# Performance work log

Measured on AMD Instinct MI355X. Metric: run time of the kernel, lower is better.

## Reference

```python
import jax, jax.numpy as jnp
import numpy as np

B = 256
NUM_CAPS = 2            # digit capsules
N_IN = 6 * 6 * 6 * 32   # 6912 input capsules
D_OUT = 16
D_IN = 8
N_ROUTING = 3           # original loops range(3 - 1) = 2 iterations
EPS = 1e-9


def squash(s):
    # squash along last axis: (|s|^2/(1+|s|^2)) * s/|s|
    n2 = jnp.sum(s * s, axis=-1, keepdims=True)
    return (n2 / (1.0 + n2)) * s / jnp.sqrt(n2 + EPS)


def setup_inputs() -> dict:
    key = jax.random.key(0)
    k1, k2 = jax.random.split(key)
    x = jax.random.normal(k1, (B, N_IN, D_IN), dtype=jnp.float32)
    W = jax.random.normal(k2, (NUM_CAPS, N_IN, D_OUT, D_IN), dtype=jnp.float32) * 0.1
    return {"x": x, "W": W}


def reference(x, W):
    # tile x over the 2 digit capsules + per-(capsule, input-capsule) matvec:
    # u_hat[b,j,n,e] = sum_d W[j,n,e,d] * x[b,n,d]   -> [B, 2, N, 16]
    u_hat = jnp.einsum('bnd,jned->bjne', x, W)
    b_logits = jnp.zeros(u_hat.shape[:3], dtype=x.dtype)  # [B, 2, N]
    v = None
    for _ in range(N_ROUTING - 1):
        c = jax.nn.softmax(b_logits, axis=1)               # softmax over the 2 capsules (dim=1 in source)
        s = jnp.einsum('bjn,bjne->bje', c, u_hat)          # [B, 2, 16]
        v = squash(s)
        b_logits = b_logits + jnp.einsum('bje,bjne->bjn', v, u_hat)
    return v
```

## Files before the change

kernel.cpp:

```cpp
#include <hip/hip_runtime.h>

#define B_ 256
#define J_ 2
#define N_ 6912
#define E_ 16
#define D_ 8
#define NPW 9
#define NB 36
#define CGX 192


__global__ __launch_bounds__(256, 3) void kpass1(const float* __restrict__ x,
                                                 const float* __restrict__ W,
                                                 float* __restrict__ partial)
{
  __shared__ float smem[9216];
  const int tid  = threadIdx.x;
  const int lane = tid & 63;
  const int wv   = __builtin_amdgcn_readfirstlane(tid >> 6);
  const int b    = blockIdx.y*64 + lane;
  const int nb0  = blockIdx.x * NB;

  const float* xp = x + ((size_t)b*N_ + nb0 + wv*NPW)*D_;
  float4 pa0 = *(const float4*)(xp + 0);
  float4 pb0 = *(const float4*)(xp + 4);
  float4 pa1 = *(const float4*)(xp + 8);
  float4 pb1 = *(const float4*)(xp + 12);

  float4 wbuf[9];
  #pragma unroll
  for (int k=0;k<9;++k){
    const int idx = k*256 + tid;
    const int j   = (idx >= 1152) ? 1 : 0;
    const int r4  = idx - j*1152;
    wbuf[k] = *(const float4*)(W + ((size_t)j*N_ + nb0)*(E_*D_) + (size_t)r4*4);
  }
  #pragma unroll
  for (int k=0;k<9;++k)
    *(float4*)(smem + (size_t)(k*256 + tid)*4) = wbuf[k];
  __syncthreads();

  float acc[32];
  #pragma unroll
  for (int i=0;i<32;++i) acc[i]=0.f;

  #pragma unroll 1
  for (int ni=0; ni<9; ++ni){
    const float4 va = pa0, vb = pb0;
    pa0 = pa1; pb0 = pb1;
    if (ni < 7){
      pa1 = *(const float4*)(xp + (ni+2)*8);
      pb1 = *(const float4*)(xp + (ni+2)*8 + 4);
    }
    const int nl = wv*NPW + ni;
    #pragma unroll
    for (int j=0;j<J_;++j){
      const float* wp = smem + (j*NB + nl)*(E_*D_);
      #pragma unroll
      for (int e=0;e<E_;++e){
        const float4 wa = *(const float4*)(wp + e*8);
        const float4 wb = *(const float4*)(wp + e*8 + 4);
        float a = acc[j*16+e];
        a = fmaf(wa.x, va.x, a); a = fmaf(wa.y, va.y, a);
        a = fmaf(wa.z, va.z, a); a = fmaf(wa.w, va.w, a);
        a = fmaf(wb.x, vb.x, a); a = fmaf(wb.y, vb.y, a);
        a = fmaf(wb.z, vb.z, a); a = fmaf(wb.w, vb.w, a);
        acc[j*16+e] = a;
      }
    }
  }

  __syncthreads();
  #pragma unroll
  for (int i=0;i<32;++i) smem[tid*33 + i] = acc[i];
  __syncthreads();
  const int bl = tid >> 2;
  const int i0 = (tid & 3) * 8;
  float v[8];
  #pragma unroll
  for (int k=0;k<8;++k){
    float s = 0.f;
    #pragma unroll
    for (int w=0; w<4; ++w) s += smem[(w*64 + bl)*33 + i0 + k];
    v[k] = s;
  }
  float* dst = partial + (size_t)(blockIdx.x*4 + blockIdx.y)*2048 + bl*32 + i0;
  *(float4*)(dst)     = make_float4(v[0],v[1],v[2],v[3]);
  *(float4*)(dst + 4) = make_float4(v[4],v[5],v[6],v[7]);
}

__global__ __launch_bounds__(256, 3) void kpass2(const float* __restrict__ x,
                                                 const float* __restrict__ W,
                                                 const float* __restrict__ v1,
                                                 float* __restrict__ partial)
{
  __shared__ float smem[9216];
  const int tid  = threadIdx.x;
  const int lane = tid & 63;
  const int wv   = __builtin_amdgcn_readfirstlane(tid >> 6);
  const int b    = blockIdx.y*64 + lane;
  const int nb0  = blockIdx.x * NB;

  const float* xp = x + ((size_t)b*N_ + nb0 + wv*NPW)*D_;
  float4 pa0 = *(const float4*)(xp + 0);
  float4 pb0 = *(const float4*)(xp + 4);
  float4 pa1 = *(const float4*)(xp + 8);
  float4 pb1 = *(const float4*)(xp + 12);

  float4 wbuf[9];
  #pragma unroll
  for (int k=0;k<9;++k){
    const int idx = k*256 + tid;
    const int j   = (idx >= 1152) ? 1 : 0;
    const int r4  = idx - j*1152;
    wbuf[k] = *(const float4*)(W + ((size_t)j*N_ + nb0)*(E_*D_) + (size_t)r4*4);
  }
  #pragma unroll
  for (int k=0;k<9;++k)
    *(float4*)(smem + (size_t)(k*256 + tid)*4) = wbuf[k];

  float vv[32];
  {
    const float4* vp = (const float4*)(v1 + (size_t)b*32);
    #pragma unroll
    for (int q=0;q<8;++q){
      const float4 t4 = vp[q];
      vv[q*4+0]=t4.x; vv[q*4+1]=t4.y; vv[q*4+2]=t4.z; vv[q*4+3]=t4.w;
    }
  }
  __syncthreads();

  float acc[32];
  #pragma unroll
  for (int i=0;i<32;++i) acc[i]=0.f;

  #pragma unroll 1
  for (int ni=0; ni<9; ++ni){
    const float4 va = pa0, vb = pb0;
    pa0 = pa1; pb0 = pb1;
    if (ni < 7){
      pa1 = *(const float4*)(xp + (ni+2)*8);
      pb1 = *(const float4*)(xp + (ni+2)*8 + 4);
    }
    const int nl = wv*NPW + ni;
    float u[32];
    #pragma unroll
    for (int j=0;j<J_;++j){
      const float* wp = smem + (j*NB + nl)*(E_*D_);
      #pragma unroll
      for (int e=0;e<E_;++e){
        const float4 wa = *(const float4*)(wp + e*8);
        const float4 wb = *(const float4*)(wp + e*8 + 4);
        float a;
        a = wa.x*va.x;           a = fmaf(wa.y, va.y, a);
        a = fmaf(wa.z, va.z, a); a = fmaf(wa.w, va.w, a);
        a = fmaf(wb.x, vb.x, a); a = fmaf(wb.y, vb.y, a);
        a = fmaf(wb.z, vb.z, a); a = fmaf(wb.w, vb.w, a);
        u[j*16+e] = a;
      }
    }
    float l0=0.f, l1=0.f;
    #pragma unroll
    for (int e=0;e<E_;++e){
      l0 = fmaf(vv[e],    u[e],    l0);
      l1 = fmaf(vv[16+e], u[16+e], l1);
    }
    const float c0 = 1.f/(1.f + __expf(l1 - l0));
    const float c1 = 1.f - c0;
    #pragma unroll
    for (int e=0;e<E_;++e){
      acc[e]    = fmaf(c0, u[e],    acc[e]);
      acc[16+e] = fmaf(c1, u[16+e], acc[16+e]);
    }
  }

  __syncthreads();
  #pragma unroll
  for (int i=0;i<32;++i) smem[tid*33 + i] = acc[i];
  __syncthreads();
  const int bl = tid >> 2;
  const int i0 = (tid & 3) * 8;
  float v[8];
  #pragma unroll
  for (int k=0;k<8;++k){
    float s = 0.f;
    #pragma unroll
    for (int w=0; w<4; ++w) s += smem[(w*64 + bl)*33 + i0 + k];
    v[k] = s;
  }
  float* dst = partial + (size_t)(blockIdx.x*4 + blockIdx.y)*2048 + bl*32 + i0;
  *(float4*)(dst)     = make_float4(v[0],v[1],v[2],v[3]);
  *(float4*)(dst + 4) = make_float4(v[4],v[5],v[6],v[7]);
}

template<bool HALF>
__global__ __launch_bounds__(256) void kred(const float* __restrict__ partial,
                                            float* __restrict__ dst)
{
  const int t = blockIdx.x*256 + threadIdx.x;
  const int btile = t >> 11, q = t & 2047;
  const float* p = partial + (size_t)btile*2048 + q;
  float s = 0.f;
  #pragma unroll 8
  for (int cx=0; cx<CGX; ++cx) s += p[(size_t)cx*8192];
  if (HALF) s *= 0.5f;
  float n2 = s*s;
  #pragma unroll
  for (int m=1; m<16; m<<=1) n2 += __shfl_xor(n2, m);
  const float f = (n2/(1.f+n2)) * rsqrtf(n2 + 1e-9f);
  dst[t] = s * f;
}

#define NT 512
__global__ __launch_bounds__(NT) void kmono(const float* __restrict__ x,
                                            const float* __restrict__ W,
                                            float* __restrict__ out)
{
  const int b    = blockIdx.x;
  const int tid  = threadIdx.x;
  const int wv   = tid >> 6;
  const int lane = tid & 63;
  __shared__ float wred[8*33];
  __shared__ float vsh[32];

  float acc[32];
  #pragma unroll
  for (int i=0;i<32;++i) acc[i]=0.f;
  for (int n = tid; n < N_; n += NT){
    const float4 xa = *(const float4*)(x + ((size_t)b*N_ + n)*D_);
    const float4 xb = *(const float4*)(x + ((size_t)b*N_ + n)*D_ + 4);
    #pragma unroll
    for (int j=0;j<J_;++j){
      const float* wp = W + ((size_t)j*N_ + n)*(E_*D_);
      #pragma unroll
      for (int e=0;e<E_;++e){
        const float4 wa = *(const float4*)(wp + e*8);
        const float4 wb = *(const float4*)(wp + e*8 + 4);
        float a = acc[j*16+e];
        a = fmaf(wa.x,xa.x,a); a = fmaf(wa.y,xa.y,a); a = fmaf(wa.z,xa.z,a); a = fmaf(wa.w,xa.w,a);
        a = fmaf(wb.x,xb.x,a); a = fmaf(wb.y,xb.y,a); a = fmaf(wb.z,xb.z,a); a = fmaf(wb.w,xb.w,a);
        acc[j*16+e] = a;
      }
    }
  }
  #pragma unroll
  for (int i=0;i<32;++i){
    float v = acc[i];
    #pragma unroll
    for (int off=32; off; off>>=1) v += __shfl_xor(v, off);
    acc[i] = v;
  }
  if (lane == 0){
    #pragma unroll
    for (int i=0;i<32;++i) wred[wv*33 + i] = acc[i];
  }
  __syncthreads();
  if (tid < 32){
    float s = 0.f;
    #pragma unroll
    for (int w=0;w<8;++w) s += wred[w*33 + tid];
    wred[tid] = 0.5f * s;
  }
  __syncthreads();
  if (tid < 32){
    const int j = tid >> 4; float n2 = 0.f;
    #pragma unroll
    for (int e=0;e<16;++e){ const float sv = wred[j*16+e]; n2 = fmaf(sv,sv,n2); }
    vsh[tid] = wred[tid] * (n2/(1.f+n2)) * rsqrtf(n2 + 1e-9f);
  }
  __syncthreads();
  float vv[32];
  #pragma unroll
  for (int i=0;i<32;++i) vv[i] = vsh[i];

  #pragma unroll
  for (int i=0;i<32;++i) acc[i]=0.f;
  for (int n = tid; n < N_; n += NT){
    const float4 xa = *(const float4*)(x + ((size_t)b*N_ + n)*D_);
    const float4 xb = *(const float4*)(x + ((size_t)b*N_ + n)*D_ + 4);
    float u[32];
    #pragma unroll
    for (int j=0;j<J_;++j){
      const float* wp = W + ((size_t)j*N_ + n)*(E_*D_);
      #pragma unroll
      for (int e=0;e<E_;++e){
        const float4 wa = *(const float4*)(wp + e*8);
        const float4 wb = *(const float4*)(wp + e*8 + 4);
        float a;
        a = wa.x*xa.x; a = fmaf(wa.y,xa.y,a); a = fmaf(wa.z,xa.z,a); a = fmaf(wa.w,xa.w,a);
        a = fmaf(wb.x,xb.x,a); a = fmaf(wb.y,xb.y,a); a = fmaf(wb.z,xb.z,a); a = fmaf(wb.w,xb.w,a);
        u[j*16+e] = a;
      }
    }
    float l0=0.f, l1=0.f;
    #pragma unroll
    for (int e=0;e<16;++e){ l0 = fmaf(vv[e],u[e],l0); l1 = fmaf(vv[16+e],u[16+e],l1); }
    const float c0 = 1.f/(1.f + __expf(l1 - l0));
    const float c1 = 1.f - c0;
    #pragma unroll
    for (int e=0;e<16;++e){ acc[e] = fmaf(c0,u[e],acc[e]); acc[16+e] = fmaf(c1,u[16+e],acc[16+e]); }
  }
  #pragma unroll
  for (int i=0;i<32;++i){
    float v = acc[i];
    #pragma unroll
    for (int off=32; off; off>>=1) v += __shfl_xor(v, off);
    acc[i] = v;
  }
  __syncthreads();
  if (lane == 0){
    #pragma unroll
    for (int i=0;i<32;++i) wred[wv*33 + i] = acc[i];
  }
  __syncthreads();
  if (tid < 32){
    float s = 0.f;
    #pragma unroll
    for (int w=0;w<8;++w) s += wred[w*33 + tid];
    wred[tid] = s;
  }
  __syncthreads();
  if (tid < 32){
    const int j = tid >> 4; float n2 = 0.f;
    #pragma unroll
    for (int e=0;e<16;++e){ const float sv = wred[j*16+e]; n2 = fmaf(sv,sv,n2); }
    out[(size_t)b*32 + tid] = wred[tid] * (n2/(1.f+n2)) * rsqrtf(n2 + 1e-9f);
  }
}

extern "C" void kernel_launch(void* const* d_in, const int* in_sizes, int n_in,
                              void* d_out, int out_size, void* d_ws, size_t ws_size,
                              hipStream_t stream)
{
  const float* x = (const float*)d_in[0];
  const float* W = (const float*)d_in[1];
  if (n_in >= 2 && in_sizes[0] < in_sizes[1]){
    x = (const float*)d_in[1]; W = (const float*)d_in[0];
  }
  float* out = (float*)d_out;

  const size_t need_main = (size_t)(8192 + 768*2048) * sizeof(float);

  if (ws_size >= need_main){
    float* wsf     = (float*)d_ws;
    float* v1      = wsf;
    float* partial = wsf + 8192;
    kpass1<<<dim3(CGX,4), 256, 0, stream>>>(x, W, partial);
    kred<true ><<<32, 256, 0, stream>>>(partial, v1);
    kpass2<<<dim3(CGX,4), 256, 0, stream>>>(x, W, v1, partial);
    kred<false><<<32, 256, 0, stream>>>(partial, out);
  } else {
    kmono<<<B_, NT, 0, stream>>>(x, W, out);
  }
}
```

Measured before the change: 162.7 us.

## Remap threads to output element and batch so each wave covers all input capsules

Threads are reassigned so that each lane owns one output element e for 4 batch rows, and each wave walks all 36 input capsules of the block, instead of each lane owning a batch row with 32 accumulators over 9 capsules per wave. This drops the cross-wave shared-memory reduction and its barriers and lowers register pressure. In pass 2 the agreement dot product over e becomes a DPP row reduction across 16 lanes, and the divide becomes a fast reciprocal. The cost is that x rows are now loaded redundantly by 16 lanes (broadcast loads), and the per-iteration shared-memory weight reads are strided by e, which may cause bank conflicts.

```diff
diff --git a/kernel.cpp b/kernel.cpp
--- a/kernel.cpp
+++ b/kernel.cpp
@@ -5,9 +5,17 @@
 #define N_ 6912
 #define E_ 16
 #define D_ 8
-#define NPW 9
 #define NB 36
 #define CGX 192
+#define BSTR (4*N_*D_)
+
+__device__ __forceinline__ float dpp_row_add16(float v){
+  v += __int_as_float(__builtin_amdgcn_update_dpp(0, __float_as_int(v), 0xB1,  0xF, 0xF, true));
+  v += __int_as_float(__builtin_amdgcn_update_dpp(0, __float_as_int(v), 0x4E,  0xF, 0xF, true));
+  v += __int_as_float(__builtin_amdgcn_update_dpp(0, __float_as_int(v), 0x141, 0xF, 0xF, true));
+  v += __int_as_float(__builtin_amdgcn_update_dpp(0, __float_as_int(v), 0x140, 0xF, 0xF, true));
+  return v;
+}
 
 
 __global__ __launch_bounds__(256, 3) void kpass1(const float* __restrict__ x,
@@ -18,14 +26,9 @@
   const int tid  = threadIdx.x;
   const int lane = tid & 63;
   const int wv   = __builtin_amdgcn_readfirstlane(tid >> 6);
-  const int b    = blockIdx.y*64 + lane;
+  const int e    = lane & 15;
+  const int blo  = lane >> 4;
   const int nb0  = blockIdx.x * NB;
-
-  const float* xp = x + ((size_t)b*N_ + nb0 + wv*NPW)*D_;
-  float4 pa0 = *(const float4*)(xp + 0);
-  float4 pb0 = *(const float4*)(xp + 4);
-  float4 pa1 = *(const float4*)(xp + 8);
-  float4 pb1 = *(const float4*)(xp + 12);
 
   float4 wbuf[9];
   #pragma unroll
@@ -38,55 +41,58 @@
   #pragma unroll
   for (int k=0;k<9;++k)
     *(float4*)(smem + (size_t)(k*256 + tid)*4) = wbuf[k];
-  __syncthreads();
-
-  float acc[32];
-  #pragma unroll
-  for (int i=0;i<32;++i) acc[i]=0.f;
-
+
+  const int b0 = blockIdx.y*64 + wv*16 + blo;
+  const float* xp = x + ((size_t)b0*N_ + nb0)*D_;
+
+  float4 xa[4], xb[4];
+  #pragma unroll
+  for (int k=0;k<4;++k){
+    xa[k] = *(const float4*)(xp + (size_t)k*BSTR);
+    xb[k] = *(const float4*)(xp + (size_t)k*BSTR + 4);
+  }
+  __syncthreads();
+
+  float acc0[4] = {0,0,0,0}, acc1[4] = {0,0,0,0};
   #pragma unroll 1
-  for (int ni=0; ni<9; ++ni){
-    const float4 va = pa0, vb = pb0;
-    pa0 = pa1; pb0 = pb1;
-    if (ni < 7){
-      pa1 = *(const float4*)(xp + (ni+2)*8);
-      pb1 = *(const float4*)(xp + (ni+2)*8 + 4);
-    }
-    const int nl = wv*NPW + ni;
-    #pragma unroll
-    for (int j=0;j<J_;++j){
-      const float* wp = smem + (j*NB + nl)*(E_*D_);
+  for (int ni=0; ni<NB; ++ni){
+    float4 ca[4], cb[4];
+    #pragma unroll
+    for (int k=0;k<4;++k){ ca[k]=xa[k]; cb[k]=xb[k]; }
+    if (ni+1 < NB){
       #pragma unroll
-      for (int e=0;e<E_;++e){
-        const float4 wa = *(const float4*)(wp + e*8);
-        const float4 wb = *(const float4*)(wp + e*8 + 4);
-        float a = acc[j*16+e];
-        a = fmaf(wa.x, va.x, a); a = fmaf(wa.y, va.y, a);
-        a = fmaf(wa.z, va.z, a); a = fmaf(wa.w, va.w, a);
-        a = fmaf(wb.x, vb.x, a); a = fmaf(wb.y, vb.y, a);
-        a = fmaf(wb.z, vb.z, a); a = fmaf(wb.w, vb.w, a);
-        acc[j*16+e] = a;
+      for (int k=0;k<4;++k){
+        xa[k] = *(const float4*)(xp + (size_t)k*BSTR + (ni+1)*8);
+        xb[k] = *(const float4*)(xp + (size_t)k*BSTR + (ni+1)*8 + 4);
       }
     }
-  }
-
-  __syncthreads();
-  #pragma unroll
-  for (int i=0;i<32;++i) smem[tid*33 + i] = acc[i];
-  __syncthreads();
-  const int bl = tid >> 2;
-  const int i0 = (tid & 3) * 8;
-  float v[8];
-  #pragma unroll
-  for (int k=0;k<8;++k){
-    float s = 0.f;
-    #pragma unroll
-    for (int w=0; w<4; ++w) s += smem[(w*64 + bl)*33 + i0 + k];
-    v[k] = s;
-  }
-  float* dst = partial + (size_t)(blockIdx.x*4 + blockIdx.y)*2048 + bl*32 + i0;
-  *(float4*)(dst)     = make_float4(v[0],v[1],v[2],v[3]);
-  *(float4*)(dst + 4) = make_float4(v[4],v[5],v[6],v[7]);
+    const float* wp0 = smem + ni*(E_*D_) + e*8;
+    const float4 wa0 = *(const float4*)(wp0);
+    const float4 wb0 = *(const float4*)(wp0 + 4);
+    const float4 wa1 = *(const float4*)(wp0 + NB*(E_*D_));
+    const float4 wb1 = *(const float4*)(wp0 + NB*(E_*D_) + 4);
+    #pragma unroll
+    for (int k=0;k<4;++k){
+      float a0 = acc0[k], a1 = acc1[k];
+      a0 = fmaf(wa0.x, ca[k].x, a0); a0 = fmaf(wa0.y, ca[k].y, a0);
+      a0 = fmaf(wa0.z, ca[k].z, a0); a0 = fmaf(wa0.w, ca[k].w, a0);
+      a0 = fmaf(wb0.x, cb[k].x, a0); a0 = fmaf(wb0.y, cb[k].y, a0);
+      a0 = fmaf(wb0.z, cb[k].z, a0); a0 = fmaf(wb0.w, cb[k].w, a0);
+      a1 = fmaf(wa1.x, ca[k].x, a1); a1 = fmaf(wa1.y, ca[k].y, a1);
+      a1 = fmaf(wa1.z, ca[k].z, a1); a1 = fmaf(wa1.w, ca[k].w, a1);
+      a1 = fmaf(wb1.x, cb[k].x, a1); a1 = fmaf(wb1.y, cb[k].y, a1);
+      a1 = fmaf(wb1.z, cb[k].z, a1); a1 = fmaf(wb1.w, cb[k].w, a1);
+      acc0[k] = a0; acc1[k] = a1;
+    }
+  }
+
+  float* dst = partial + (size_t)(blockIdx.x*4 + blockIdx.y)*2048
+             + (wv*16 + blo)*32 + e;
+  #pragma unroll
+  for (int k=0;k<4;++k){
+    dst[k*128]      = acc0[k];
+    dst[k*128 + 16] = acc1[k];
+  }
 }
 
 __global__ __launch_bounds__(256, 3) void kpass2(const float* __restrict__ x,
@@ -98,14 +104,9 @@
   const int tid  = threadIdx.x;
   const int lane = tid & 63;
   const int wv   = __builtin_amdgcn_readfirstlane(tid >> 6);
-  const int b    = blockIdx.y*64 + lane;
+  const int e    = lane & 15;
+  const int blo  = lane >> 4;
   const int nb0  = blockIdx.x * NB;
-
-  const float* xp = x + ((size_t)b*N_ + nb0 + wv*NPW)*D_;
-  float4 pa0 = *(const float4*)(xp + 0);
-  float4 pb0 = *(const float4*)(xp + 4);
-  float4 pa1 = *(const float4*)(xp + 8);
-  float4 pb1 = *(const float4*)(xp + 12);
 
   float4 wbuf[9];
   #pragma unroll
@@ -119,78 +120,72 @@
   for (int k=0;k<9;++k)
     *(float4*)(smem + (size_t)(k*256 + tid)*4) = wbuf[k];
 
-  float vv[32];
-  {
-    const float4* vp = (const float4*)(v1 + (size_t)b*32);
-    #pragma unroll
-    for (int q=0;q<8;++q){
-      const float4 t4 = vp[q];
-      vv[q*4+0]=t4.x; vv[q*4+1]=t4.y; vv[q*4+2]=t4.z; vv[q*4+3]=t4.w;
-    }
-  }
-  __syncthreads();
-
-  float acc[32];
-  #pragma unroll
-  for (int i=0;i<32;++i) acc[i]=0.f;
-
+  const int b0 = blockIdx.y*64 + wv*16 + blo;
+  const float* xp = x + ((size_t)b0*N_ + nb0)*D_;
+
+  float4 xa[4], xb[4];
+  #pragma unroll
+  for (int k=0;k<4;++k){
+    xa[k] = *(const float4*)(xp + (size_t)k*BSTR);
+    xb[k] = *(const float4*)(xp + (size_t)k*BSTR + 4);
+  }
+  float vj0[4], vj1[4];
+  #pragma unroll
+  for (int k=0;k<4;++k){
+    vj0[k] = v1[(size_t)(b0 + 4*k)*32 + e];
+    vj1[k] = v1[(size_t)(b0 + 4*k)*32 + 16 + e];
+  }
+  __syncthreads();
+
+  float acc0[4] = {0,0,0,0}, acc1[4] = {0,0,0,0};
   #pragma unroll 1
-  for (int ni=0; ni<9; ++ni){
-    const float4 va = pa0, vb = pb0;
-    pa0 = pa1; pb0 = pb1;
-    if (ni < 7){
-      pa1 = *(const float4*)(xp + (ni+2)*8);
-      pb1 = *(const float4*)(xp + (ni+2)*8 + 4);
-    }
-    const int nl = wv*NPW + ni;
-    float u[32];
-    #pragma unroll
-    for (int j=0;j<J_;++j){
-      const float* wp = smem + (j*NB + nl)*(E_*D_);
+  for (int ni=0; ni<NB; ++ni){
+    float4 ca[4], cb[4];
+    #pragma unroll
+    for (int k=0;k<4;++k){ ca[k]=xa[k]; cb[k]=xb[k]; }
+    if (ni+1 < NB){
       #pragma unroll
-      for (int e=0;e<E_;++e){
-        const float4 wa = *(const float4*)(wp + e*8);
-        const float4 wb = *(const float4*)(wp + e*8 + 4);
-        float a;
-        a = wa.x*va.x;           a = fmaf(wa.y, va.y, a);
-        a = fmaf(wa.z, va.z, a); a = fmaf(wa.w, va.w, a);
-        a = fmaf(wb.x, vb.x, a); a = fmaf(wb.y, vb.y, a);
-        a = fmaf(wb.z, vb.z, a); a = fmaf(wb.w, vb.w, a);
-        u[j*16+e] = a;
+      for (int k=0;k<4;++k){
+        xa[k] = *(const float4*)(xp + (size_t)k*BSTR + (ni+1)*8);
+        xb[k] = *(const float4*)(xp + (size_t)k*BSTR + (ni+1)*8 + 4);
       }
     }
-    float l0=0.f, l1=0.f;
-    #pragma unroll
-    for (int e=0;e<E_;++e){
-      l0 = fmaf(vv[e],    u[e],    l0);
-      l1 = fmaf(vv[16+e], u[16+e], l1);
-    }
-    const float c0 = 1.f/(1.f + __expf(l1 - l0));
-    const float c1 = 1.f - c0;
-    #pragma unroll
-    for (int e=0;e<E_;++e){
-      acc[e]    = fmaf(c0, u[e],    acc[e]);
-      acc[16+e] = fmaf(c1, u[16+e], acc[16+e]);
-    }
-  }
-
-  __syncthreads();
-  #pragma unroll
-  for (int i=0;i<32;++i) smem[tid*33 + i] = acc[i];
-  __syncthreads();
-  const int bl = tid >> 2;
-  const int i0 = (tid & 3) * 8;
-  float v[8];
-  #pragma unroll
-  for (int k=0;k<8;++k){
-    float s = 0.f;
-    #pragma unroll
-    for (int w=0; w<4; ++w) s += smem[(w*64 + bl)*33 + i0 + k];
-    v[k] = s;
-  }
-  float* dst = partial + (size_t)(blockIdx.x*4 + blockIdx.y)*2048 + bl*32 + i0;
-  *(float4*)(dst)     = make_float4(v[0],v[1],v[2],v[3]);
-  *(float4*)(dst + 4) = make_float4(v[4],v[5],v[6],v[7]);
+    const float* wp0 = smem + ni*(E_*D_) + e*8;
+    const float4 wa0 = *(const float4*)(wp0);
+    const float4 wb0 = *(const float4*)(wp0 + 4);
+    const float4 wa1 = *(const float4*)(wp0 + NB*(E_*D_));
+    const float4 wb1 = *(const float4*)(wp0 + NB*(E_*D_) + 4);
+
+    float u0[4], u1[4];
+    #pragma unroll
+    for (int k=0;k<4;++k){
+      float a0, a1;
+      a0 = wa0.x*ca[k].x;        a0 = fmaf(wa0.y, ca[k].y, a0);
+      a0 = fmaf(wa0.z, ca[k].z, a0); a0 = fmaf(wa0.w, ca[k].w, a0);
+      a0 = fmaf(wb0.x, cb[k].x, a0); a0 = fmaf(wb0.y, cb[k].y, a0);
+      a0 = fmaf(wb0.z, cb[k].z, a0); a0 = fmaf(wb0.w, cb[k].w, a0);
+      a1 = wa1.x*ca[k].x;        a1 = fmaf(wa1.y, ca[k].y, a1);
+      a1 = fmaf(wa1.z, ca[k].z, a1); a1 = fmaf(wa1.w, ca[k].w, a1);
+      a1 = fmaf(wb1.x, cb[k].x, a1); a1 = fmaf(wb1.y, cb[k].y, a1);
+      a1 = fmaf(wb1.z, cb[k].z, a1); a1 = fmaf(wb1.w, cb[k].w, a1);
+      u0[k] = a0; u1[k] = a1;
+    }
+    #pragma unroll
+    for (int k=0;k<4;++k){
+      const float d  = dpp_row_add16(fmaf(vj1[k], u1[k], -(vj0[k]*u0[k])));
+      const float c0 = __builtin_amdgcn_rcpf(1.f + __expf(d));
+      acc0[k] = fmaf(c0,       u0[k], acc0[k]);
+      acc1[k] = fmaf(1.f - c0, u1[k], acc1[k]);
+    }
+  }
+
+  float* dst = partial + (size_t)(blockIdx.x*4 + blockIdx.y)*2048
+             + (wv*16 + blo)*32 + e;
+  #pragma unroll
+  for (int k=0;k<4;++k){
+    dst[k*128]      = acc0[k];
+    dst[k*128 + 16] = acc1[k];
+  }
 }
 
 template<bool HALF>
```

After: 170.5 us. 4.8% more time.
